# Kernel tuning notes

Measured on AMD Instinct MI355X. Metric: run time of the kernel, lower is better.

The kernel has to match this reference:

```python
import jax, jax.numpy as jnp
import numpy as np

B = 16384
LEN_VOCAB = 2048
IPD_VOCAB = 2048
EBDIN = 32


def setup_inputs() -> dict:
    key = jax.random.key(0)
    ks = jax.random.split(key, 11)
    return {
        "x": jax.random.randint(ks[0], (B, 1, 2), 0, LEN_VOCAB, dtype=jnp.int64)
        if jax.config.jax_enable_x64 else jax.random.randint(ks[0], (B, 1, 2), 0, LEN_VOCAB),
        "lenebdLUT": jax.random.normal(ks[1], (LEN_VOCAB, EBDIN), jnp.float32),
        "ipdebdLUT": jax.random.normal(ks[2], (IPD_VOCAB, EBDIN), jnp.float32),
        "S1": jax.random.normal(ks[3], (15, 2, 15), jnp.float32),
        "H1": jax.random.normal(ks[4], (45, 4096), jnp.float32),
        "T1": jax.random.normal(ks[5], (15, 15), jnp.float32),
        "LUT1": jax.random.normal(ks[6], (5, 4096, 32), jnp.float32),
        "S2": jax.random.normal(ks[7], (1, 2, 15), jnp.float32),
        "H2": jax.random.normal(ks[8], (15, 16), jnp.float32),
        "T2": jax.random.normal(ks[9], (1, 15), jnp.float32),
        "LUT2": jax.random.normal(ks[10], (1, 16, 32), jnp.float32),
    }


def _forward(x, lenebdLUT, ipdebdLUT, S1, H1, T1, LUT1, S2, H2, T2, LUT2):
    batch = x.shape[0]
    # embedding lookups, summed: [B,1,32] -> flatten to [B,32] (seq==1)
    e = (lenebdLUT[x[:, :, 0]] + ipdebdLUT[x[:, :, 1]]).reshape(-1, EBDIN)
    ebd = e
    # ---- newMM on first 30 features ----
    a = jnp.einsum('bcd,cdk->bck', e[:, :30].reshape(-1, 15, 2), S1)  # [B,15,15]
    a = a - T1 - 1e-4
    t = jnp.tanh(a)
    a = jax.lax.stop_gradient(jnp.sign(a) - t) + t  # straight-through sign
    a = a.reshape(-1, 5, 45)
    scores1 = jnp.einsum('bcd,dk->bck', a, H1)       # [B,5,4096]
    idx1 = jnp.argmax(scores1, axis=-1)              # [B,5]
    # one_hot(argmax) @ LUT == per-codebook gather
    x1 = LUT1[jnp.arange(5)[None, :], idx1]          # [B,5,32]
    # ---- MM_final on last 2 features ----
    b = jnp.einsum('bcd,cdk->bck', e[:, 30:32].reshape(-1, 1, 2), S2)  # [B,1,15]
    b = b - T2
    b = jnp.where(b == 0, jnp.float32(-1.0), jnp.sign(b))  # x[x==0]=-1; sign(x)
    scores2 = jnp.einsum('bcd,dk->bck', b, H2)       # [B,1,16]
    idx2 = jnp.argmax(scores2, axis=-1)              # [B,1]
    x2 = LUT2[jnp.arange(1)[None, :], idx2]          # [B,1,32]
    x2 = jnp.sum(x2, axis=1).reshape(batch, 1, 32)
    reconstruct = jnp.concatenate([x1, x2], axis=1).sum(axis=1)  # [B,32]
    return reconstruct, ebd


def reference(x, lenebdLUT, ipdebdLUT, S1, H1, T1, LUT1, S2, H2, T2, LUT2):
    return _forward(x, lenebdLUT, ipdebdLUT, S1, H1, T1, LUT1, S2, H2, T2, LUT2)
```

## Files before the change

kernel.cpp:

```cpp
#include <hip/hip_runtime.h>

#define B_TOT 16384
#define NPAIR (B_TOT*5)
#define NPT32 (NPAIR/32)
#define NKG   8
#define KTPG  16
#define KTB   9216
#define PHB   (2*KTB)

typedef __attribute__((ext_vector_type(8))) short bf16x8;
typedef __attribute__((ext_vector_type(16))) float f32x16;

struct alignas(8) us4 { unsigned short x, y, z, w; };

__device__ inline unsigned short f2bf(float f) {
    unsigned u = __builtin_bit_cast(unsigned, f);
    unsigned r = u + 0x7fffu + ((u >> 16) & 1u);
    return (unsigned short)(r >> 16);
}
__device__ inline float bf2f(unsigned short b) {
    unsigned u = ((unsigned)b) << 16;
    return __builtin_bit_cast(float, u);
}
__device__ inline float max3f(float a, float b, float c) {
    return fmaxf(fmaxf(a, b), c);
}

__global__ __launch_bounds__(64) void kprep(const float* __restrict__ H1,
                                            unsigned short* __restrict__ Abuf) {
    int blk = blockIdx.x;
    int kt = blk / 9, rem = blk - kt*9;
    int s = rem / 3, q = rem - s*3;
    int l = threadIdx.x;
    int h = l >> 5;
    int row = kt*32 + (l & 31);
    unsigned short o[8];
#pragma unroll
    for (int j = 0; j < 8; ++j) {
        int d = 16*s + 4*h + ((j < 4) ? j : (j + 4));
        float v = (d < 45) ? H1[(size_t)d*4096 + row] : 0.f;
        unsigned short b = 0;
        for (int qq = 0; qq <= q; ++qq) { b = f2bf(v); v -= bf2f(b); }
        o[j] = b;
    }
    unsigned short* dst = Abuf + (size_t)blk*512 + l*8;
    *(us4*)(dst)     = us4{o[0], o[1], o[2], o[3]};
    *(us4*)(dst + 4) = us4{o[4], o[5], o[6], o[7]};
}

__global__ __launch_bounds__(64) void k1_fused(
    const int* __restrict__ x,
    const float* __restrict__ lenLUT, const float* __restrict__ ipdLUT,
    const float* __restrict__ S1, const float* __restrict__ T1,
    const float* __restrict__ S2, const float* __restrict__ H2,
    const float* __restrict__ T2, const float* __restrict__ LUT2,
    float* __restrict__ out, float* __restrict__ p2vec,
    unsigned short* __restrict__ Bbuf) {
    int b = blockIdx.x * blockDim.x + threadIdx.x;
    if (b >= B_TOT) return;
    int x0 = x[2*b], x1 = x[2*b+1];
    float e[32];
    const float4* l4 = (const float4*)(lenLUT + (size_t)x0*32);
    const float4* i4 = (const float4*)(ipdLUT + (size_t)x1*32);
    float4* o4 = (float4*)(out + (size_t)B_TOT*32 + (size_t)b*32);
#pragma unroll
    for (int j = 0; j < 8; ++j) {
        float4 a = l4[j], c = i4[j];
        float4 sv; sv.x=a.x+c.x; sv.y=a.y+c.y; sv.z=a.z+c.z; sv.w=a.w+c.w;
        e[4*j+0]=sv.x; e[4*j+1]=sv.y; e[4*j+2]=sv.z; e[4*j+3]=sv.w;
        o4[j] = sv;
    }
#pragma unroll
    for (int c = 0; c < 5; ++c) {
        unsigned short sg[48];
#pragma unroll
        for (int d45 = 0; d45 < 45; ++d45) {
            int gi = c*45 + d45;
            int c15 = gi / 15, k = gi - c15*15;
            float a = e[2*c15] * S1[(2*c15)*15 + k] + e[2*c15+1] * S1[(2*c15+1)*15 + k];
            a = a - T1[c15*15 + k];
            a = a - 1e-4f;
            sg[d45] = (a > 0.f) ? (unsigned short)0x3F80u
                    : ((a < 0.f) ? (unsigned short)0xBF80u : (unsigned short)0);
        }
        sg[45] = 0; sg[46] = 0; sg[47] = 0;
        int p = b*5 + c, P = p >> 5, col = p & 31;
        unsigned short* base = Bbuf + (size_t)P*1536;
#pragma unroll
        for (int s = 0; s < 3; ++s) {
            unsigned short* blk = base + s*512;
            *(us4*)(blk + col*8)          = us4{sg[16*s+0],  sg[16*s+1],  sg[16*s+2],  sg[16*s+3]};
            *(us4*)(blk + col*8 + 4)      = us4{sg[16*s+8],  sg[16*s+9],  sg[16*s+10], sg[16*s+11]};
            *(us4*)(blk + (col+32)*8)     = us4{sg[16*s+4],  sg[16*s+5],  sg[16*s+6],  sg[16*s+7]};
            *(us4*)(blk + (col+32)*8 + 4) = us4{sg[16*s+12], sg[16*s+13], sg[16*s+14], sg[16*s+15]};
        }
    }
    float e30 = e[30], e31 = e[31];
    float sb[15];
#pragma unroll
    for (int k = 0; k < 15; ++k) {
        float bb = e30 * S2[k] + e31 * S2[15 + k];
        bb = bb - T2[k];
        sb[k] = (bb > 0.f) ? 1.f : -1.f;
    }
    float best = -3.4e38f; int bi = 0;
#pragma unroll
    for (int k2 = 0; k2 < 16; ++k2) {
        float sc = 0.f;
#pragma unroll
        for (int d = 0; d < 15; ++d) sc = fmaf(sb[d], H2[d*16 + k2], sc);
        if (sc > best) { best = sc; bi = k2; }
    }
    const float4* lr = (const float4*)(LUT2 + (size_t)bi*32);
    float4* pv = (float4*)(p2vec + (size_t)b*32);
#pragma unroll
    for (int j = 0; j < 8; ++j) pv[j] = lr[j];
}

__global__ __launch_bounds__(256, 3) void k2m(
    const unsigned short* __restrict__ Abuf,
    const unsigned short* __restrict__ Bbuf,
    float* __restrict__ pval, int* __restrict__ pidx) {
    const int bid = blockIdx.x;
    const int kg = bid & 7;
    const int pg = bid >> 3;
    const int tid = threadIdx.x;
    const int w = tid >> 6, l = tid & 63;
    const int pt0 = pg*8 + w*2;

    __shared__ __align__(16) char lds[2][PHB];

    bf16x8 Bf[2][3];
#pragma unroll
    for (int i = 0; i < 2; ++i)
#pragma unroll
        for (int s = 0; s < 3; ++s)
            Bf[i][s] = *(const bf16x8*)(Bbuf + ((size_t)(pt0+i)*3 + s)*512 + l*8);

    float bv16[2][16];
    float V[2] = {-3.4e38f, -3.4e38f};
    int bkt[2] = {0, 0};
#pragma unroll
    for (int i = 0; i < 2; ++i)
#pragma unroll
        for (int r = 0; r < 16; ++r) bv16[i][r] = -3.4e38f;

    const char* Asrc = (const char*)Abuf + (size_t)kg*KTPG*KTB;

#pragma unroll
    for (int r = 0; r < 5; ++r) {
        int idx = tid + r*256;
        if (idx < PHB/16)
            __builtin_amdgcn_global_load_lds(
                (const __attribute__((address_space(1))) unsigned int*)(Asrc + (size_t)idx*16),
                (__attribute__((address_space(3))) unsigned int*)(&lds[0][idx*16]),
                16, 0, 0);
    }
    __syncthreads();

    f32x16 zf;
#pragma unroll
    for (int r = 0; r < 16; ++r) zf[r] = 0.f;

    for (int ph = 0; ph < 8; ++ph) {
        const int cur = ph & 1;
        if (ph < 7) {
            const char* src = Asrc + (size_t)(ph+1)*PHB;
#pragma unroll
            for (int r = 0; r < 5; ++r) {
                int idx = tid + r*256;
                if (idx < PHB/16)
                    __builtin_amdgcn_global_load_lds(
                        (const __attribute__((address_space(1))) unsigned int*)(src + (size_t)idx*16),
                        (__attribute__((address_space(3))) unsigned int*)(&lds[cur^1][idx*16]),
                        16, 0, 0);
            }
        }
#pragma unroll
        for (int kt2 = 0; kt2 < 2; ++kt2) {
            const int ktl = ph*2 + kt2;
            const char* ab = &lds[cur][kt2*KTB + l*16];
            bf16x8 A[9];
#pragma unroll
            for (int f = 0; f < 9; ++f)
                A[f] = *(const bf16x8*)(ab + f*1024);

            f32x16 acc0, acc1;
            acc0 = __builtin_amdgcn_mfma_f32_32x32x16_bf16(A[0], Bf[0][0], zf, 0, 0, 0);
            acc1 = __builtin_amdgcn_mfma_f32_32x32x16_bf16(A[0], Bf[1][0], zf, 0, 0, 0);
#pragma unroll
            for (int s = 0; s < 3; ++s)
#pragma unroll
                for (int q = 0; q < 3; ++q) {
                    if (s == 0 && q == 0) continue;
                    const int f = s*3 + q;
                    acc0 = __builtin_amdgcn_mfma_f32_32x32x16_bf16(A[f], Bf[0][s], acc0, 0, 0, 0);
                    acc1 = __builtin_amdgcn_mfma_f32_32x32x16_bf16(A[f], Bf[1][s], acc1, 0, 0, 0);
                }
#pragma unroll
            for (int i = 0; i < 2; ++i) {
                const f32x16& a = (i == 0) ? acc0 : acc1;
                float m0 = max3f(a[0],  a[1],  a[2]);
                float m1 = max3f(a[3],  a[4],  a[5]);
                float m2 = max3f(a[6],  a[7],  a[8]);
                float m3 = max3f(a[9],  a[10], a[11]);
                float m4 = max3f(a[12], a[13], a[14]);
                float m5 = max3f(m0, m1, a[15]);
                float m6 = max3f(m2, m3, m4);
                float t  = fmaxf(m5, m6);
                bkt[i] = (t > V[i]) ? ktl : bkt[i];
                V[i] = fmaxf(V[i], t);
#pragma unroll
                for (int r = 0; r < 16; ++r)
                    bv16[i][r] = fmaxf(bv16[i][r], a[r]);
            }
        }
        __syncthreads();
    }

    const int h = l >> 5;
#pragma unroll
    for (int i = 0; i < 2; ++i) {
        int rb = 0;
#pragma unroll
        for (int r = 15; r >= 0; --r)
            rb = (bv16[i][r] == V[i]) ? r : rb;
        int kk = kg*512 + bkt[i]*32 + (rb & 3) + ((rb >> 2) << 3) + (h << 2);
        float v = V[i];
        float ov = __shfl_xor(v, 32);
        int   ok = __shfl_xor(kk, 32);
        if (ov > v || (ov == v && ok < kk)) { v = ov; kk = ok; }
        if (l < 32) {
            int pair = (pt0 + i)*32 + l;
            pval[(size_t)pair*NKG + kg] = v;
            pidx[(size_t)pair*NKG + kg] = kk;
        }
    }
}

__global__ __launch_bounds__(64) void k3_final(
    const float* __restrict__ pval, const int* __restrict__ pidx,
    const float* __restrict__ LUT1, const float* __restrict__ p2vec,
    float* __restrict__ out) {
    int b = blockIdx.x * blockDim.x + threadIdx.x;
    if (b >= B_TOT) return;
    float4 r[8];
    const float4* pv = (const float4*)(p2vec + (size_t)b*32);
#pragma unroll
    for (int j = 0; j < 8; ++j) r[j] = pv[j];
#pragma unroll
    for (int c = 0; c < 5; ++c) {
        size_t pair = (size_t)b*5 + c;
        const float4* pv4 = (const float4*)(pval + pair*NKG);
        const int4*   pi4 = (const int4*)(pidx + pair*NKG);
        float4 v0 = pv4[0], v1 = pv4[1];
        int4   i0 = pi4[0], i1 = pi4[1];
        float vv[8] = {v0.x, v0.y, v0.z, v0.w, v1.x, v1.y, v1.z, v1.w};
        int   ii[8] = {i0.x, i0.y, i0.z, i0.w, i1.x, i1.y, i1.z, i1.w};
        float bvv = vv[0]; int bk = ii[0];
#pragma unroll
        for (int q = 1; q < 8; ++q) {
            if (vv[q] > bvv) { bvv = vv[q]; bk = ii[q]; }
        }
        const float4* lr = (const float4*)(LUT1 + ((size_t)c*4096 + bk)*32);
#pragma unroll
        for (int j = 0; j < 8; ++j) {
            float4 t = lr[j];
            r[j].x += t.x; r[j].y += t.y; r[j].z += t.z; r[j].w += t.w;
        }
    }
    float4* o4 = (float4*)(out + (size_t)b*32);
#pragma unroll
    for (int j = 0; j < 8; ++j) o4[j] = r[j];
}

extern "C" void kernel_launch(void* const* d_in, const int* in_sizes, int n_in,
                              void* d_out, int out_size, void* d_ws, size_t ws_size,
                              hipStream_t stream) {
    const int*   x      = (const int*)d_in[0];
    const float* lenLUT = (const float*)d_in[1];
    const float* ipdLUT = (const float*)d_in[2];
    const float* S1     = (const float*)d_in[3];
    const float* H1     = (const float*)d_in[4];
    const float* T1     = (const float*)d_in[5];
    const float* LUT1   = (const float*)d_in[6];
    const float* S2     = (const float*)d_in[7];
    const float* H2     = (const float*)d_in[8];
    const float* T2     = (const float*)d_in[9];
    const float* LUT2   = (const float*)d_in[10];
    float* out = (float*)d_out;

    char* ws = (char*)d_ws;
    unsigned short* Abuf = (unsigned short*)ws;
    size_t off = (size_t)1152*1024;
    unsigned short* Bbuf = (unsigned short*)(ws + off);
    off += (size_t)NPT32*1536*2;
    float* p2vec = (float*)(ws + off);
    off += (size_t)B_TOT*32*4;
    float* pval  = (float*)(ws + off);
    off += (size_t)NPAIR*NKG*4;
    int*   pidx  = (int*)(ws + off);

    kprep<<<dim3(1152), dim3(64), 0, stream>>>(H1, Abuf);
    k1_fused<<<dim3(B_TOT/64), dim3(64), 0, stream>>>(
        x, lenLUT, ipdLUT, S1, T1, S2, H2, T2, LUT2, out, p2vec, Bbuf);
    k2m<<<dim3(2560), dim3(256), 0, stream>>>(Abuf, Bbuf, pval, pidx);
    k3_final<<<dim3(B_TOT/64), dim3(64), 0, stream>>>(
        pval, pidx, LUT1, p2vec, out);
}
```

Baseline: 104.4 us.

## Merge prep and front kernels into one launch and widen per-thread parallelism

Folds the H1 bf16-split prep kernel and the embedding/sign kernel into a single launch whose block ranges do different jobs. The sign computation now uses one thread per (batch, codebook) pair instead of one per batch row, and the embedding copy plus the second codebook run in their own block range. k3_final now uses eight threads per row, each handling one float4 lane, and k2m's occupancy hint goes from 3 to 4 blocks. The aim is to cut one launch and expose more parallelism in the small front and back kernels. In exchange, the embedding rows and pair indices are read redundantly across threads, and the tighter k2m bound may cause register spills.

```diff
diff --git a/kernel.cpp b/kernel.cpp
--- a/kernel.cpp
+++ b/kernel.cpp
@@ -8,6 +8,10 @@
 #define KTB   9216
 #define PHB   (2*KTB)
 
+#define PREP_BLKS 288
+#define SIGN_BLKS 320
+#define EMBD_BLKS 64
+
 typedef __attribute__((ext_vector_type(8))) short bf16x8;
 typedef __attribute__((ext_vector_type(16))) float f32x16;
 
@@ -26,65 +30,69 @@
     return fmaxf(fmaxf(a, b), c);
 }
 
-__global__ __launch_bounds__(64) void kprep(const float* __restrict__ H1,
-                                            unsigned short* __restrict__ Abuf) {
-    int blk = blockIdx.x;
-    int kt = blk / 9, rem = blk - kt*9;
-    int s = rem / 3, q = rem - s*3;
-    int l = threadIdx.x;
-    int h = l >> 5;
-    int row = kt*32 + (l & 31);
-    unsigned short o[8];
-#pragma unroll
-    for (int j = 0; j < 8; ++j) {
-        int d = 16*s + 4*h + ((j < 4) ? j : (j + 4));
-        float v = (d < 45) ? H1[(size_t)d*4096 + row] : 0.f;
-        unsigned short b = 0;
-        for (int qq = 0; qq <= q; ++qq) { b = f2bf(v); v -= bf2f(b); }
-        o[j] = b;
-    }
-    unsigned short* dst = Abuf + (size_t)blk*512 + l*8;
-    *(us4*)(dst)     = us4{o[0], o[1], o[2], o[3]};
-    *(us4*)(dst + 4) = us4{o[4], o[5], o[6], o[7]};
-}
-
-__global__ __launch_bounds__(64) void k1_fused(
+__global__ __launch_bounds__(256) void kfront(
     const int* __restrict__ x,
     const float* __restrict__ lenLUT, const float* __restrict__ ipdLUT,
-    const float* __restrict__ S1, const float* __restrict__ T1,
+    const float* __restrict__ S1, const float* __restrict__ H1,
+    const float* __restrict__ T1,
     const float* __restrict__ S2, const float* __restrict__ H2,
     const float* __restrict__ T2, const float* __restrict__ LUT2,
     float* __restrict__ out, float* __restrict__ p2vec,
-    unsigned short* __restrict__ Bbuf) {
-    int b = blockIdx.x * blockDim.x + threadIdx.x;
-    if (b >= B_TOT) return;
-    int x0 = x[2*b], x1 = x[2*b+1];
-    float e[32];
-    const float4* l4 = (const float4*)(lenLUT + (size_t)x0*32);
-    const float4* i4 = (const float4*)(ipdLUT + (size_t)x1*32);
-    float4* o4 = (float4*)(out + (size_t)B_TOT*32 + (size_t)b*32);
-#pragma unroll
-    for (int j = 0; j < 8; ++j) {
-        float4 a = l4[j], c = i4[j];
-        float4 sv; sv.x=a.x+c.x; sv.y=a.y+c.y; sv.z=a.z+c.z; sv.w=a.w+c.w;
-        e[4*j+0]=sv.x; e[4*j+1]=sv.y; e[4*j+2]=sv.z; e[4*j+3]=sv.w;
-        o4[j] = sv;
-    }
-#pragma unroll
-    for (int c = 0; c < 5; ++c) {
+    unsigned short* __restrict__ Abuf, unsigned short* __restrict__ Bbuf) {
+    const int bid = blockIdx.x;
+    const int tid = threadIdx.x;
+
+    if (bid < PREP_BLKS) {
+        int blk = bid * 4 + (tid >> 6);
+        int kt = blk / 9, rem = blk - kt*9;
+        int s = rem / 3, q = rem - s*3;
+        int l = tid & 63;
+        int h = l >> 5;
+        int row = kt*32 + (l & 31);
+        unsigned short o[8];
+#pragma unroll
+        for (int j = 0; j < 8; ++j) {
+            int d = 16*s + 4*h + ((j < 4) ? j : (j + 4));
+            float v = (d < 45) ? H1[(size_t)d*4096 + row] : 0.f;
+            unsigned short bb = 0;
+            for (int qq = 0; qq <= q; ++qq) { bb = f2bf(v); v -= bf2f(bb); }
+            o[j] = bb;
+        }
+        unsigned short* dst = Abuf + (size_t)blk*512 + l*8;
+        *(us4*)(dst)     = us4{o[0], o[1], o[2], o[3]};
+        *(us4*)(dst + 4) = us4{o[4], o[5], o[6], o[7]};
+        return;
+    }
+
+    if (bid < PREP_BLKS + SIGN_BLKS) {
+        int p = (bid - PREP_BLKS) * 256 + tid;
+        int b = p / 5;
+        int c = p - b * 5;
+        int x0 = x[2*b], x1 = x[2*b+1];
+        float e[6];
+        const float2* l2 = (const float2*)(lenLUT + (size_t)x0*32 + 6*c);
+        const float2* i2 = (const float2*)(ipdLUT + (size_t)x1*32 + 6*c);
+#pragma unroll
+        for (int t = 0; t < 3; ++t) {
+            float2 a = l2[t], d = i2[t];
+            e[2*t]   = a.x + d.x;
+            e[2*t+1] = a.y + d.y;
+        }
         unsigned short sg[48];
 #pragma unroll
-        for (int d45 = 0; d45 < 45; ++d45) {
-            int gi = c*45 + d45;
-            int c15 = gi / 15, k = gi - c15*15;
-            float a = e[2*c15] * S1[(2*c15)*15 + k] + e[2*c15+1] * S1[(2*c15+1)*15 + k];
-            a = a - T1[c15*15 + k];
-            a = a - 1e-4f;
-            sg[d45] = (a > 0.f) ? (unsigned short)0x3F80u
-                    : ((a < 0.f) ? (unsigned short)0xBF80u : (unsigned short)0);
+        for (int t = 0; t < 3; ++t) {
+            int c15 = 3*c + t;
+#pragma unroll
+            for (int k = 0; k < 15; ++k) {
+                float a = e[2*t] * S1[(2*c15)*15 + k] + e[2*t+1] * S1[(2*c15+1)*15 + k];
+                a = a - T1[c15*15 + k];
+                a = a - 1e-4f;
+                sg[t*15+k] = (a > 0.f) ? (unsigned short)0x3F80u
+                           : ((a < 0.f) ? (unsigned short)0xBF80u : (unsigned short)0);
+            }
         }
         sg[45] = 0; sg[46] = 0; sg[47] = 0;
-        int p = b*5 + c, P = p >> 5, col = p & 31;
+        int P = p >> 5, col = p & 31;
         unsigned short* base = Bbuf + (size_t)P*1536;
 #pragma unroll
         for (int s = 0; s < 3; ++s) {
@@ -94,30 +102,47 @@
             *(us4*)(blk + (col+32)*8)     = us4{sg[16*s+4],  sg[16*s+5],  sg[16*s+6],  sg[16*s+7]};
             *(us4*)(blk + (col+32)*8 + 4) = us4{sg[16*s+12], sg[16*s+13], sg[16*s+14], sg[16*s+15]};
         }
-    }
-    float e30 = e[30], e31 = e[31];
-    float sb[15];
-#pragma unroll
-    for (int k = 0; k < 15; ++k) {
-        float bb = e30 * S2[k] + e31 * S2[15 + k];
-        bb = bb - T2[k];
-        sb[k] = (bb > 0.f) ? 1.f : -1.f;
-    }
-    float best = -3.4e38f; int bi = 0;
-#pragma unroll
-    for (int k2 = 0; k2 < 16; ++k2) {
-        float sc = 0.f;
-#pragma unroll
-        for (int d = 0; d < 15; ++d) sc = fmaf(sb[d], H2[d*16 + k2], sc);
-        if (sc > best) { best = sc; bi = k2; }
-    }
-    const float4* lr = (const float4*)(LUT2 + (size_t)bi*32);
-    float4* pv = (float4*)(p2vec + (size_t)b*32);
-#pragma unroll
-    for (int j = 0; j < 8; ++j) pv[j] = lr[j];
-}
-
-__global__ __launch_bounds__(256, 3) void k2m(
+        return;
+    }
+
+    {
+        int b = (bid - PREP_BLKS - SIGN_BLKS) * 256 + tid;
+        if (b >= B_TOT) return;
+        int x0 = x[2*b], x1 = x[2*b+1];
+        const float4* l4 = (const float4*)(lenLUT + (size_t)x0*32);
+        const float4* i4 = (const float4*)(ipdLUT + (size_t)x1*32);
+        float4* o4 = (float4*)(out + (size_t)B_TOT*32 + (size_t)b*32);
+        float e30 = 0.f, e31 = 0.f;
+#pragma unroll
+        for (int j = 0; j < 8; ++j) {
+            float4 a = l4[j], c = i4[j];
+            float4 sv; sv.x=a.x+c.x; sv.y=a.y+c.y; sv.z=a.z+c.z; sv.w=a.w+c.w;
+            o4[j] = sv;
+            if (j == 7) { e30 = sv.z; e31 = sv.w; }
+        }
+        float sb[15];
+#pragma unroll
+        for (int k = 0; k < 15; ++k) {
+            float bb = e30 * S2[k] + e31 * S2[15 + k];
+            bb = bb - T2[k];
+            sb[k] = (bb > 0.f) ? 1.f : -1.f;
+        }
+        float best = -3.4e38f; int bi = 0;
+#pragma unroll
+        for (int k2 = 0; k2 < 16; ++k2) {
+            float sc = 0.f;
+#pragma unroll
+            for (int d = 0; d < 15; ++d) sc = fmaf(sb[d], H2[d*16 + k2], sc);
+            if (sc > best) { best = sc; bi = k2; }
+        }
+        const float4* lr = (const float4*)(LUT2 + (size_t)bi*32);
+        float4* pv = (float4*)(p2vec + (size_t)b*32);
+#pragma unroll
+        for (int j = 0; j < 8; ++j) pv[j] = lr[j];
+    }
+}
+
+__global__ __launch_bounds__(256, 4) void k2m(
     const unsigned short* __restrict__ Abuf,
     const unsigned short* __restrict__ Bbuf,
     float* __restrict__ pval, int* __restrict__ pidx) {
@@ -238,16 +263,14 @@
     }
 }
 
-__global__ __launch_bounds__(64) void k3_final(
+__global__ __launch_bounds__(256) void k3_final(
     const float* __restrict__ pval, const int* __restrict__ pidx,
     const float* __restrict__ LUT1, const float* __restrict__ p2vec,
     float* __restrict__ out) {
-    int b = blockIdx.x * blockDim.x + threadIdx.x;
+    int t = blockIdx.x * 256 + threadIdx.x;
+    int b = t >> 3, j = t & 7;
     if (b >= B_TOT) return;
-    float4 r[8];
-    const float4* pv = (const float4*)(p2vec + (size_t)b*32);
-#pragma unroll
-    for (int j = 0; j < 8; ++j) r[j] = pv[j];
+    float4 r = ((const float4*)(p2vec + (size_t)b*32))[j];
 #pragma unroll
     for (int c = 0; c < 5; ++c) {
         size_t pair = (size_t)b*5 + c;
@@ -262,16 +285,10 @@
         for (int q = 1; q < 8; ++q) {
             if (vv[q] > bvv) { bvv = vv[q]; bk = ii[q]; }
         }
-        const float4* lr = (const float4*)(LUT1 + ((size_t)c*4096 + bk)*32);
-#pragma unroll
-        for (int j = 0; j < 8; ++j) {
-            float4 t = lr[j];
-            r[j].x += t.x; r[j].y += t.y; r[j].z += t.z; r[j].w += t.w;
-        }
-    }
-    float4* o4 = (float4*)(out + (size_t)b*32);
-#pragma unroll
-    for (int j = 0; j < 8; ++j) o4[j] = r[j];
+        float4 tl = ((const float4*)(LUT1 + ((size_t)c*4096 + bk)*32))[j];
+        r.x += tl.x; r.y += tl.y; r.z += tl.z; r.w += tl.w;
+    }
+    ((float4*)(out + (size_t)b*32))[j] = r;
 }
 
 extern "C" void kernel_launch(void* const* d_in, const int* in_sizes, int n_in,
@@ -301,10 +318,9 @@
     off += (size_t)NPAIR*NKG*4;
     int*   pidx  = (int*)(ws + off);
 
-    kprep<<<dim3(1152), dim3(64), 0, stream>>>(H1, Abuf);
-    k1_fused<<<dim3(B_TOT/64), dim3(64), 0, stream>>>(
-        x, lenLUT, ipdLUT, S1, T1, S2, H2, T2, LUT2, out, p2vec, Bbuf);
+    kfront<<<dim3(PREP_BLKS + SIGN_BLKS + EMBD_BLKS), dim3(256), 0, stream>>>(
+        x, lenLUT, ipdLUT, S1, H1, T1, S2, H2, T2, LUT2, out, p2vec, Abuf, Bbuf);
     k2m<<<dim3(2560), dim3(256), 0, stream>>>(Abuf, Bbuf, pval, pidx);
-    k3_final<<<dim3(B_TOT/64), dim3(64), 0, stream>>>(
+    k3_final<<<dim3(B_TOT*8/256), dim3(256), 0, stream>>>(
         pval, pidx, LUT1, p2vec, out);
 }
```

After: 141.9 us. +35.9%, slower.
